# Performance work log

Hardware: AMD Instinct MI355X
Metric: run time of the kernel (lower is better)

## Reference

```python
import jax, jax.numpy as jnp
import numpy as np

B = 4096          # batch_size * world_size
D = 256           # embedding dim
TEMP = 0.5        # temperature
EPS = 1e-8


def setup_inputs() -> dict:
    key = jax.random.key(0)
    k1, k2 = jax.random.split(key)
    z_i = jax.random.normal(k1, (B, D), dtype=jnp.float32)
    z_j = jax.random.normal(k2, (B, D), dtype=jnp.float32)
    return {"z_i": z_i, "z_j": z_j}


def reference(z_i, z_j):
    N = 2 * B
    z = jnp.concatenate([z_i, z_j], axis=0)                      # [N, D]
    # cosine similarity = normalized dot products (normalize + GEMM)
    norm = jnp.sqrt(jnp.sum(z * z, axis=-1, keepdims=True))
    zn = z / jnp.maximum(norm, EPS)
    sim = (zn @ zn.T) / TEMP                                     # [N, N]
    # positives: pairs (i, i+B) and (i+B, i)
    idx = jnp.arange(N)
    pos = sim[idx, (idx + B) % N]                                # [N]
    # CE with label 0 over [pos, negatives]; the candidate set equals the
    # full sim row minus the diagonal (pos is re-included), so:
    sim_masked = jnp.where(jnp.eye(N, dtype=bool), -jnp.inf, sim)
    lse = jax.nn.logsumexp(sim_masked, axis=1)                   # [N]
    loss = jnp.sum(lse - pos) / N                                # reduction='sum' then /N
    return loss
```

## Files before the change

### kernel.cpp

```cpp
#include <hip/hip_runtime.h>
#include <hip/hip_bf16.h>
#include <cmath>

#define B_SZ 4096
#define N_SZ 8192
#define D_SZ 256
#define EPS 1e-8f
#define EXPC 0.01127105500694503f
#define EXPB -2.8853900817779268f

typedef __attribute__((ext_vector_type(4))) float f32x4;
typedef __attribute__((ext_vector_type(4))) int   i32x4;
typedef __attribute__((ext_vector_type(8))) int   i32x8;


__global__ __launch_bounds__(256) void prep_kernel(const float* __restrict__ zi,
                                                   const float* __restrict__ zj,
                                                   char* __restrict__ znb,
                                                   float* __restrict__ pos) {
    const int wave = threadIdx.x >> 6, lane = threadIdx.x & 63;
    const int i = blockIdx.x * 4 + wave;
    float4 a = reinterpret_cast<const float4*>(zi + (size_t)i * D_SZ)[lane];
    float4 b = reinterpret_cast<const float4*>(zj + (size_t)i * D_SZ)[lane];
    float ssa = a.x * a.x + a.y * a.y + a.z * a.z + a.w * a.w;
    float ssb = b.x * b.x + b.y * b.y + b.z * b.z + b.w * b.w;
    float dab = a.x * b.x + a.y * b.y + a.z * b.z + a.w * b.w;
    #pragma unroll
    for (int off = 32; off; off >>= 1) {
        ssa += __shfl_xor(ssa, off, 64);
        ssb += __shfl_xor(ssb, off, 64);
        dab += __shfl_xor(dab, off, 64);
    }
    const float invna = 1.0f / fmaxf(sqrtf(ssa), EPS);
    const float invnb = 1.0f / fmaxf(sqrtf(ssb), EPS);
    if (lane == 0) {
        float p = dab * invna * invnb * 2.0f;
        pos[i] = p;
        pos[i + B_SZ] = p;
    }
    const float sa = invna * 16.0f, sb = invnb * 16.0f;
    const int koff = (lane >> 2) * 1024 + (lane & 3) * 4;
    {
        int pk = __builtin_amdgcn_cvt_pk_fp8_f32(a.x * sa, a.y * sa, 0, false);
        pk     = __builtin_amdgcn_cvt_pk_fp8_f32(a.z * sa, a.w * sa, pk, true);
        *reinterpret_cast<int*>(znb + (size_t)(i >> 6) * 16384 + koff + (i & 63) * 16) = pk;
    }
    {
        const int r = i + B_SZ;
        int pk = __builtin_amdgcn_cvt_pk_fp8_f32(b.x * sb, b.y * sb, 0, false);
        pk     = __builtin_amdgcn_cvt_pk_fp8_f32(b.z * sb, b.w * sb, pk, true);
        *reinterpret_cast<int*>(znb + (size_t)(r >> 6) * 16384 + koff + (r & 63) * 16) = pk;
    }
}

__global__ __launch_bounds__(512, 4) void simlse_kernel(const char* __restrict__ znb,
                                                        float* __restrict__ partial) {
    const int t = threadIdx.x;
    const int wave = t >> 6, lane = t & 63;

    int bid = blockIdx.x, rt = 0;
    #pragma unroll 1
    for (; rt < 32; ++rt) {
        int cnt = 32 - rt;
        if (bid < cnt) break;
        bid -= cnt;
    }
    const int chunk = rt + bid;
    const bool offdiag = (rt != chunk);
    __shared__ float cs[8][256];

    const int rl = lane & 15;
    const int kg = lane >> 4;
    const int i0 = rt * 256 + wave * 32;

    const char* ap = znb + (size_t)(rt * 4 + (wave >> 1)) * 16384 +
                     (wave & 1) * 512 + rl * 16;
    i32x8 afrag[2][2];
    #pragma unroll
    for (int g = 0; g < 2; ++g)
        #pragma unroll
        for (int kc = 0; kc < 2; ++kc) {
            i32x4 lo = *reinterpret_cast<const i32x4*>(
                ap + (kc * 8 + kg * 2) * 1024 + g * 256);
            i32x4 hi = *reinterpret_cast<const i32x4*>(
                ap + (kc * 8 + kg * 2 + 1) * 1024 + g * 256);
            afrag[g][kc] = __builtin_shufflevector(lo, hi, 0, 1, 2, 3, 4, 5, 6, 7);
        }

    float s_acc[2][4];
    #pragma unroll
    for (int g = 0; g < 2; ++g)
        #pragma unroll
        for (int r = 0; r < 4; ++r) s_acc[g][r] = 0.0f;

    const char* bp0 = znb + (size_t)chunk * 4 * 16384 + kg * 2048 + rl * 16;

    i32x4 nb0 = *reinterpret_cast<const i32x4*>(bp0);
    i32x4 nb1 = *reinterpret_cast<const i32x4*>(bp0 + 1024);
    i32x4 nb2 = *reinterpret_cast<const i32x4*>(bp0 + 8192);
    i32x4 nb3 = *reinterpret_cast<const i32x4*>(bp0 + 9216);

    i32x8 bf0, bf1;
    f32x4 accA[2], accB[2];

    #define PREP_B(F)                                                             \
        {                                                                         \
            bf0 = __builtin_shufflevector(nb0, nb1, 0, 1, 2, 3, 4, 5, 6, 7);      \
            bf1 = __builtin_shufflevector(nb2, nb3, 0, 1, 2, 3, 4, 5, 6, 7);      \
            if ((F) < 15) {                                                       \
                const char* bq = bp0 + (((F) + 1) >> 2) * 16384 +                 \
                                 (((F) + 1) & 3) * 256;                           \
                nb0 = *reinterpret_cast<const i32x4*>(bq);                        \
                nb1 = *reinterpret_cast<const i32x4*>(bq + 1024);                 \
                nb2 = *reinterpret_cast<const i32x4*>(bq + 8192);                 \
                nb3 = *reinterpret_cast<const i32x4*>(bq + 9216);                 \
            }                                                                     \
        }

    #define MFMA4(ACC)                                                            \
        {                                                                         \
            _Pragma("unroll")                                                     \
            for (int g = 0; g < 2; ++g) ACC[g] = (f32x4){0.f, 0.f, 0.f, 0.f};     \
            _Pragma("unroll")                                                     \
            for (int g = 0; g < 2; ++g)                                           \
                asm("v_mfma_f32_16x16x128_f8f6f4 %0, %1, %2, %0"                  \
                    : "+v"(ACC[g]) : "v"(afrag[g][0]), "v"(bf0));                 \
            _Pragma("unroll")                                                     \
            for (int g = 0; g < 2; ++g)                                           \
                asm("v_mfma_f32_16x16x128_f8f6f4 %0, %1, %2, %0"                  \
                    : "+v"(ACC[g]) : "v"(afrag[g][1]), "v"(bf1));                 \
        }

    #define EXPSUM(ACC, F)                                                        \
        {                                                                         \
            float cthr = 0.0f;                                                    \
            _Pragma("unroll")                                                     \
            for (int g = 0; g < 2; ++g)                                           \
                _Pragma("unroll")                                                 \
                for (int r = 0; r < 4; ++r) {                                     \
                    float e = __builtin_amdgcn_exp2f(fmaf(ACC[g][r], EXPC, EXPB)); \
                    s_acc[g][r] += e;                                             \
                    cthr += e;                                                    \
                }                                                                 \
            cthr += __shfl_xor(cthr, 16, 64);                                     \
            cthr += __shfl_xor(cthr, 32, 64);                                     \
            if (offdiag && lane < 16)                                             \
                cs[wave][((F) >> 2) * 64 + ((F) & 3) * 16 + rl] = cthr;           \
        }

    PREP_B(0);
    MFMA4(accA);
    #pragma unroll 1
    for (int fo = 0; fo < 7; ++fo) {
        const int f1 = 2 * fo + 1, f2 = 2 * fo + 2;
        PREP_B(f1); MFMA4(accB);
        asm volatile("s_nop 7");
        EXPSUM(accA, f1 - 1);
        PREP_B(f2); MFMA4(accA);
        asm volatile("s_nop 7");
        EXPSUM(accB, f2 - 1);
    }
    PREP_B(15); MFMA4(accB);
    asm volatile("s_nop 7");
    EXPSUM(accA, 14);
    asm volatile("s_nop 7");
    EXPSUM(accB, 15);

    #pragma unroll
    for (int g = 0; g < 2; ++g)
        #pragma unroll
        for (int r = 0; r < 4; ++r) {
            float v = s_acc[g][r];
            #pragma unroll
            for (int off = 1; off < 16; off <<= 1) v += __shfl_xor(v, off, 64);
            if (rl == 0)
                partial[chunk * N_SZ + i0 + g * 16 + kg * 4 + r] = v;
        }

    if (offdiag) {
        __syncthreads();
        if (t < 256) {
            float v = 0.0f;
            #pragma unroll
            for (int w = 0; w < 8; ++w) v += cs[w][t];
            partial[rt * N_SZ + chunk * 256 + t] = v;
        }
    }
    #undef PREP_B
    #undef MFMA4
    #undef EXPSUM
}

__global__ __launch_bounds__(256) void rowsum_kernel(const float* __restrict__ partial,
                                                     const float* __restrict__ pos,
                                                     float* __restrict__ bpart) {
    const int row = blockIdx.x * 256 + threadIdx.x;
    float s = -1.0f;
    #pragma unroll
    for (int c = 0; c < 32; ++c) s += partial[c * N_SZ + row];
    float acc = 2.0f + logf(s) - pos[row];
    #pragma unroll
    for (int off = 32; off; off >>= 1) acc += __shfl_xor(acc, off, 64);
    __shared__ float w[4];
    if ((threadIdx.x & 63) == 0) w[threadIdx.x >> 6] = acc;
    __syncthreads();
    if (threadIdx.x == 0) bpart[blockIdx.x] = w[0] + w[1] + w[2] + w[3];
}

__global__ __launch_bounds__(64) void finsum_kernel(const float* __restrict__ bpart,
                                                    float* __restrict__ out) {
    float v = threadIdx.x < 32 ? bpart[threadIdx.x] : 0.0f;
    #pragma unroll
    for (int off = 32; off; off >>= 1) v += __shfl_xor(v, off, 64);
    if (threadIdx.x == 0) out[0] = v / (float)N_SZ;
}

extern "C" void kernel_launch(void* const* d_in, const int* in_sizes, int n_in,
                              void* d_out, int out_size, void* d_ws, size_t ws_size,
                              hipStream_t stream) {
    const float* zi = (const float*)d_in[0];
    const float* zj = (const float*)d_in[1];

    char* ws = (char*)d_ws;
    char* znb      = ws;
    float* pos     = (float*)(ws + 2097152);
    float* partial = (float*)(ws + 2097152 + 32768);
    float* bpart   = (float*)(ws + 2097152 + 32768 + 1048576);
    float* out = (float*)d_out;

    prep_kernel<<<B_SZ / 4, 256, 0, stream>>>(zi, zj, znb, pos);
    simlse_kernel<<<528, 512, 0, stream>>>(znb, partial);
    rowsum_kernel<<<32, 256, 0, stream>>>(partial, pos, bpart);
    finsum_kernel<<<1, 64, 0, stream>>>(bpart, out);
}
```

Baseline: 33.58 us.

## Stage B tile in LDS via async global-to-LDS DMA and fuse final reduction

The simlse kernel now copies each block's 64KB B chunk into shared memory with global_load_lds DMA up front, then reads MFMA B fragments from LDS instead of register-prefetching them from global memory. The final finsum launch is removed: rowsum blocks atomically accumulate into a float and the last block writes the loss, with the accumulator and counter zeroed in prep_kernel. This removes repeated global fetches across waves and one kernel launch. The cost is 72KB of LDS per block, which limits occupancy, plus a sync before compute with no overlap of the load, and an atomic float sum whose order is nondeterministic.

```diff
diff --git a/kernel.cpp b/kernel.cpp
--- a/kernel.cpp
+++ b/kernel.cpp
@@ -13,11 +13,20 @@
 typedef __attribute__((ext_vector_type(4))) int   i32x4;
 typedef __attribute__((ext_vector_type(8))) int   i32x8;
 
+__device__ __forceinline__ void dma16(const void* g, void* l) {
+    __builtin_amdgcn_global_load_lds(
+        (const __attribute__((address_space(1))) unsigned int*)g,
+        (__attribute__((address_space(3))) unsigned int*)l, 16, 0, 0);
+}
+
 
 __global__ __launch_bounds__(256) void prep_kernel(const float* __restrict__ zi,
                                                    const float* __restrict__ zj,
                                                    char* __restrict__ znb,
-                                                   float* __restrict__ pos) {
+                                                   float* __restrict__ pos,
+                                                   float* __restrict__ accf,
+                                                   unsigned* __restrict__ counter) {
+    if (blockIdx.x == 0 && threadIdx.x == 0) { *accf = 0.0f; *counter = 0u; }
     const int wave = threadIdx.x >> 6, lane = threadIdx.x & 63;
     const int i = blockIdx.x * 4 + wave;
     float4 a = reinterpret_cast<const float4*>(zi + (size_t)i * D_SZ)[lane];
@@ -55,6 +64,9 @@
 
 __global__ __launch_bounds__(512, 4) void simlse_kernel(const char* __restrict__ znb,
                                                         float* __restrict__ partial) {
+    __shared__ __attribute__((aligned(16))) char blds[65536];
+    __shared__ float cs[8][256];
+
     const int t = threadIdx.x;
     const int wave = t >> 6, lane = t & 63;
 
@@ -67,11 +79,17 @@
     }
     const int chunk = rt + bid;
     const bool offdiag = (rt != chunk);
-    __shared__ float cs[8][256];
 
     const int rl = lane & 15;
     const int kg = lane >> 4;
     const int i0 = rt * 256 + wave * 32;
+
+    {
+        const char* gp = znb + (size_t)chunk * 65536 + t * 16;
+        char* lp = blds + t * 16;
+        #pragma unroll
+        for (int c = 0; c < 8; ++c) dma16(gp + c * 8192, lp + c * 8192);
+    }
 
     const char* ap = znb + (size_t)(rt * 4 + (wave >> 1)) * 16384 +
                      (wave & 1) * 512 + rl * 16;
@@ -93,28 +111,20 @@
         #pragma unroll
         for (int r = 0; r < 4; ++r) s_acc[g][r] = 0.0f;
 
-    const char* bp0 = znb + (size_t)chunk * 4 * 16384 + kg * 2048 + rl * 16;
-
-    i32x4 nb0 = *reinterpret_cast<const i32x4*>(bp0);
-    i32x4 nb1 = *reinterpret_cast<const i32x4*>(bp0 + 1024);
-    i32x4 nb2 = *reinterpret_cast<const i32x4*>(bp0 + 8192);
-    i32x4 nb3 = *reinterpret_cast<const i32x4*>(bp0 + 9216);
+    const char* bp0 = blds + kg * 2048 + rl * 16;
 
     i32x8 bf0, bf1;
     f32x4 accA[2], accB[2];
 
     #define PREP_B(F)                                                             \
         {                                                                         \
-            bf0 = __builtin_shufflevector(nb0, nb1, 0, 1, 2, 3, 4, 5, 6, 7);      \
-            bf1 = __builtin_shufflevector(nb2, nb3, 0, 1, 2, 3, 4, 5, 6, 7);      \
-            if ((F) < 15) {                                                       \
-                const char* bq = bp0 + (((F) + 1) >> 2) * 16384 +                 \
-                                 (((F) + 1) & 3) * 256;                           \
-                nb0 = *reinterpret_cast<const i32x4*>(bq);                        \
-                nb1 = *reinterpret_cast<const i32x4*>(bq + 1024);                 \
-                nb2 = *reinterpret_cast<const i32x4*>(bq + 8192);                 \
-                nb3 = *reinterpret_cast<const i32x4*>(bq + 9216);                 \
-            }                                                                     \
+            const char* bq = bp0 + ((F) >> 2) * 16384 + ((F) & 3) * 256;          \
+            i32x4 l0 = *reinterpret_cast<const i32x4*>(bq);                       \
+            i32x4 l1 = *reinterpret_cast<const i32x4*>(bq + 1024);                \
+            i32x4 l2 = *reinterpret_cast<const i32x4*>(bq + 8192);                \
+            i32x4 l3 = *reinterpret_cast<const i32x4*>(bq + 9216);                \
+            bf0 = __builtin_shufflevector(l0, l1, 0, 1, 2, 3, 4, 5, 6, 7);        \
+            bf1 = __builtin_shufflevector(l2, l3, 0, 1, 2, 3, 4, 5, 6, 7);        \
         }
 
     #define MFMA4(ACC)                                                            \
@@ -148,6 +158,8 @@
                 cs[wave][((F) >> 2) * 64 + ((F) & 3) * 16 + rl] = cthr;           \
         }
 
+    __syncthreads();
+
     PREP_B(0);
     MFMA4(accA);
     #pragma unroll 1
@@ -193,7 +205,9 @@
 
 __global__ __launch_bounds__(256) void rowsum_kernel(const float* __restrict__ partial,
                                                      const float* __restrict__ pos,
-                                                     float* __restrict__ bpart) {
+                                                     float* __restrict__ accf,
+                                                     unsigned* __restrict__ counter,
+                                                     float* __restrict__ out) {
     const int row = blockIdx.x * 256 + threadIdx.x;
     float s = -1.0f;
     #pragma unroll
@@ -204,15 +218,15 @@
     __shared__ float w[4];
     if ((threadIdx.x & 63) == 0) w[threadIdx.x >> 6] = acc;
     __syncthreads();
-    if (threadIdx.x == 0) bpart[blockIdx.x] = w[0] + w[1] + w[2] + w[3];
-}
-
-__global__ __launch_bounds__(64) void finsum_kernel(const float* __restrict__ bpart,
-                                                    float* __restrict__ out) {
-    float v = threadIdx.x < 32 ? bpart[threadIdx.x] : 0.0f;
-    #pragma unroll
-    for (int off = 32; off; off >>= 1) v += __shfl_xor(v, off, 64);
-    if (threadIdx.x == 0) out[0] = v / (float)N_SZ;
+    if (threadIdx.x == 0) {
+        atomicAdd(accf, w[0] + w[1] + w[2] + w[3]);
+        __threadfence();
+        unsigned old = atomicAdd(counter, 1u);
+        if (old == 31u) {
+            float tot = atomicAdd(accf, 0.0f);
+            out[0] = tot / (float)N_SZ;
+        }
+    }
 }
 
 extern "C" void kernel_launch(void* const* d_in, const int* in_sizes, int n_in,
@@ -222,14 +236,14 @@
     const float* zj = (const float*)d_in[1];
 
     char* ws = (char*)d_ws;
-    char* znb      = ws;
-    float* pos     = (float*)(ws + 2097152);
-    float* partial = (float*)(ws + 2097152 + 32768);
-    float* bpart   = (float*)(ws + 2097152 + 32768 + 1048576);
+    char* znb       = ws;
+    float* pos      = (float*)(ws + 2097152);
+    float* partial  = (float*)(ws + 2097152 + 32768);
+    float* accf     = (float*)(ws + 2097152 + 32768 + 1048576);
+    unsigned* counter = (unsigned*)(ws + 2097152 + 32768 + 1048576 + 4);
     float* out = (float*)d_out;
 
-    prep_kernel<<<B_SZ / 4, 256, 0, stream>>>(zi, zj, znb, pos);
+    prep_kernel<<<B_SZ / 4, 256, 0, stream>>>(zi, zj, znb, pos, accf, counter);
     simlse_kernel<<<528, 512, 0, stream>>>(znb, partial);
-    rowsum_kernel<<<32, 256, 0, stream>>>(partial, pos, bpart);
-    finsum_kernel<<<1, 64, 0, stream>>>(bpart, out);
-}
+    rowsum_kernel<<<32, 256, 0, stream>>>(partial, pos, accf, counter, out);
+}
```

Result: no change. 32.92 us (-2.0%).
